# Optimization experiments

Hardware: AMD Instinct MI355X
Metric: run time of the kernel (lower is better)

Reference implementation:

```python
import jax, jax.numpy as jnp
import numpy as np

MARGIN = 1.0  # init kwarg margin=1; hard_mining=False path


def setup_inputs() -> dict:
    key = jax.random.key(0)
    k1, k2 = jax.random.split(key)
    inputs = jax.random.normal(k1, (4096, 128), dtype=jnp.float32)
    targets = jax.random.randint(k2, (4096,), 0, 64, dtype=jnp.int64)
    return {"inputs": inputs, "targets": targets}


def reference(inputs, targets):
    n = inputs.shape[0]
    # squared pairwise distances: ||xi||^2 + ||xj||^2 - 2 xi.xj, relu'd then sqrt
    sq = jnp.sum(inputs * inputs, axis=1)                      # [n]
    d2 = jnp.maximum(sq[:, None] + sq[None, :] - 2.0 * (inputs @ inputs.T), 0.0)
    nz = d2 > 0
    dist = jnp.where(nz, jnp.sqrt(jnp.where(nz, d2, 1.0)), 0.0)  # safe sqrt, [n,n]

    eye = jnp.eye(n, dtype=bool)
    same = targets[:, None] == targets[None, :]
    pos_mask = same & ~eye            # positive pairs, diag removed
    neg_mask = ~same                  # negative pairs

    # torch code gathers neg_dist[i].nonzero(): negatives with nonzero distance
    neg_valid = neg_mask & (dist != 0.0)
    row_neg = jnp.sum(jnp.where(neg_valid, jnp.exp(MARGIN - dist), 0.0), axis=1)  # [n]

    # loop runs over upper-triangular positive pairs (diag already excluded)
    idx = jnp.arange(n)
    triu_pos = pos_mask & (idx[:, None] < idx[None, :])
    J = jnp.log(row_neg[:, None] + row_neg[None, :]) + dist    # Jij_heat
    contrib = jnp.where(triu_pos, jax.nn.relu(J) ** 2, 0.0)

    len_p = jnp.sum(pos_mask).astype(inputs.dtype)             # count over FULL pos_mask
    return jnp.sum(contrib) / len_p
```

## Files before the change

### kernel.cpp

```cpp
#include <hip/hip_runtime.h>
#include <hip/hip_bf16.h>
#include <math.h>

typedef short short8 __attribute__((ext_vector_type(8)));
typedef float f32x4 __attribute__((ext_vector_type(4)));

#define NROW 4096
#define DIM  128
#define NCLS 64
#define CCAP 512
#define MAXM 128

typedef __attribute__((address_space(3))) unsigned lds_u32;
typedef const __attribute__((address_space(1))) unsigned glb_u32;

__device__ __forceinline__ void gload16(const void* g, void* lds) {
    __builtin_amdgcn_global_load_lds((glb_u32*)g, (lds_u32*)lds, 16, 0, 0);
}

__device__ __forceinline__ unsigned short f2bf(float f) {
    unsigned u = __builtin_bit_cast(unsigned, f);
    unsigned r = (u + 0x7fffu + ((u >> 16) & 1u)) >> 16;
    return (unsigned short)r;
}

__global__ __launch_bounds__(256) void prep_kernel(const float* __restrict__ X,
        unsigned short* __restrict__ Xb, float* __restrict__ sq,
        float* __restrict__ rn, float* __restrict__ acc,
        unsigned* __restrict__ tick, int* __restrict__ ccnt)
{
    int t = threadIdx.x;
    int row = blockIdx.x * 8 + (t >> 5);
    int c = t & 31;
    float4 v = *reinterpret_cast<const float4*>(X + (size_t)row * DIM + c * 4);
    float p = v.x * v.x + v.y * v.y + v.z * v.z + v.w * v.w;
    p += __shfl_xor(p, 16, 32);
    p += __shfl_xor(p, 8, 32);
    p += __shfl_xor(p, 4, 32);
    p += __shfl_xor(p, 2, 32);
    p += __shfl_xor(p, 1, 32);
    ushort4 h;
    h.x = f2bf(v.x); h.y = f2bf(v.y); h.z = f2bf(v.z); h.w = f2bf(v.w);
    *reinterpret_cast<ushort4*>(Xb + (size_t)row * DIM + c * 4) = h;
    if (c == 0) { sq[row] = p; rn[row] = 0.0f; }
    if (blockIdx.x == 0) {
        if (t < NCLS) ccnt[t] = 0;
        if (t == 64) { acc[0] = 0.0f; acc[1] = 0.0f; }
        if (t == 65) tick[0] = 0u;
    }
}

__global__ __launch_bounds__(256) void rowneg_kernel(
        const unsigned short* __restrict__ Xb, const float* __restrict__ sq,
        const int* __restrict__ tgt, float* __restrict__ rn,
        int* __restrict__ ccnt, int* __restrict__ list)
{
    const int bi = blockIdx.y, bj = blockIdx.x;
    if (bj < bi) return;
    const int gib = bi * 64, gjb = bj * 64;

    __shared__ __align__(16) unsigned short tA[64 * 128];
    __shared__ __align__(16) unsigned short tB[64 * 128];
    __shared__ float s_sqi[64], s_sqj[64];
    __shared__ float s_cacc[4][64];
    __shared__ int   s_ti[64], s_tj[64];

    const int t = threadIdx.x;
    const int w = t >> 6, l = t & 63, lr = l & 15, lg = l >> 4;

    #pragma unroll
    for (int k = 0; k < 4; ++k) {
        int q = w * 4 + k;
        int row = q * 4 + (l >> 4);
        int c16 = l & 15;
        int sc = c16 ^ (row & 7);
        gload16(Xb + (size_t)(gib + row) * DIM + sc * 8, &tA[q * 512]);
        gload16(Xb + (size_t)(gjb + row) * DIM + sc * 8, &tB[q * 512]);
    }
    if (t < 64)       { s_sqi[t] = sq[gib + t]; s_ti[t] = tgt[gib + t]; }
    else if (t < 128) { int u = t - 64; s_sqj[u] = sq[gjb + u]; s_tj[u] = tgt[gjb + u]; }
    if (bi == bj && t >= 128 && t < 192) {
        int row = gib + (t - 128);
        int cls = tgt[row];
        int p = atomicAdd(&ccnt[cls], 1);
        if (p < CCAP) list[cls * CCAP + p] = row;
    }
    __syncthreads();

    const int arow = w * 16 + lr;
    f32x4 C[4] = {};
    #pragma unroll
    for (int ks = 0; ks < 4; ++ks) {
        int c = ks * 4 + lg;
        short8 a = *reinterpret_cast<const short8*>(&tA[arow * 128 + ((c ^ (arow & 7)) * 8)]);
        #pragma unroll
        for (int fj = 0; fj < 4; ++fj) {
            int brow = fj * 16 + lr;
            short8 b = *reinterpret_cast<const short8*>(&tB[brow * 128 + ((c ^ (brow & 7)) * 8)]);
            C[fj] = __builtin_amdgcn_mfma_f32_16x16x32_bf16(a, b, C[fj], 0, 0, 0);
        }
    }

    const int ibase = w * 16 + lg * 4;
    float sqi[4]; int ti[4];
    #pragma unroll
    for (int r = 0; r < 4; ++r) { sqi[r] = s_sqi[ibase + r]; ti[r] = s_ti[ibase + r]; }

    float racc[4] = {0.f, 0.f, 0.f, 0.f};
    float cacc[4] = {0.f, 0.f, 0.f, 0.f};
    #pragma unroll
    for (int fj = 0; fj < 4; ++fj) {
        int jl = fj * 16 + lr;
        float sqj = s_sqj[jl];
        int   tj  = s_tj[jl];
        int   gj  = gjb + jl;
        #pragma unroll
        for (int r = 0; r < 4; ++r) {
            int gi = gib + ibase + r;
            float d2 = fmaxf(sqi[r] + sqj - 2.0f * C[fj][r], 0.0f);
            float dist = __builtin_amdgcn_sqrtf(d2);
            float e = __expf(1.0f - dist);
            bool valid = (gi < gj) && (ti[r] != tj) && (d2 > 0.0f);
            e = valid ? e : 0.0f;
            racc[r] += e;
            cacc[fj] += e;
        }
    }

    #pragma unroll
    for (int r = 0; r < 4; ++r) {
        racc[r] += __shfl_xor(racc[r], 1);
        racc[r] += __shfl_xor(racc[r], 2);
        racc[r] += __shfl_xor(racc[r], 4);
        racc[r] += __shfl_xor(racc[r], 8);
    }
    if (lr == 0) {
        #pragma unroll
        for (int r = 0; r < 4; ++r) atomicAdd(&rn[gib + ibase + r], racc[r]);
    }
    #pragma unroll
    for (int fj = 0; fj < 4; ++fj) {
        cacc[fj] += __shfl_xor(cacc[fj], 16);
        cacc[fj] += __shfl_xor(cacc[fj], 32);
    }
    if (lg == 0) {
        #pragma unroll
        for (int fj = 0; fj < 4; ++fj) s_cacc[w][fj * 16 + lr] = cacc[fj];
    }
    __syncthreads();
    if (t < 64) {
        float cs = s_cacc[0][t] + s_cacc[1][t] + s_cacc[2][t] + s_cacc[3][t];
        if (cs != 0.0f) atomicAdd(&rn[gjb + t], cs);
    }
}

__global__ __launch_bounds__(256) void loss_kernel(
        const unsigned short* __restrict__ Xb, const float* __restrict__ X,
        const float* __restrict__ sq, const float* __restrict__ rn,
        const int* __restrict__ ccnt, const int* __restrict__ list,
        float* __restrict__ acc, unsigned* __restrict__ tick, float* __restrict__ out)
{
    const int c = blockIdx.x;
    int m = ccnt[c]; if (m > CCAP) m = CCAP;
    const int mm = m < MAXM ? m : MAXM;
    const int nfj = (mm + 15) >> 4;

    __shared__ __align__(16) unsigned short tX[MAXM * DIM];
    __shared__ float sqg[MAXM], rng[MAXM];
    __shared__ int   s_idx[MAXM];
    __shared__ float s_red[16];

    const int t = threadIdx.x;
    const int w = t >> 6, l = t & 63, lr = l & 15, lg = l >> 4;

    if (t < MAXM) s_idx[t] = (t < mm) ? list[c * CCAP + t] : 0;
    __syncthreads();

    if (t < MAXM) {
        int ri = s_idx[t];
        sqg[t] = (t < mm) ? sq[ri] : 0.0f;
        rng[t] = (t < mm) ? rn[ri] : 0.0f;
    }
    #pragma unroll
    for (int k = 0; k < 8; ++k) {
        int q = w * 8 + k;
        int row = q * 4 + (l >> 4);
        if (row < ((mm + 3) & ~3)) {
            int c16 = l & 15;
            int sc = c16 ^ (row & 7);
            gload16(Xb + (size_t)s_idx[row] * DIM + sc * 8, &tX[q * 512]);
        }
    }
    __syncthreads();

    f32x4 C[2][8] = {};
    #pragma unroll
    for (int ks = 0; ks < 4; ++ks) {
        int cb = ks * 4 + lg;
        short8 a[2], b[8];
        #pragma unroll
        for (int fi = 0; fi < 2; ++fi) {
            int row = w * 32 + fi * 16 + lr;
            a[fi] = *reinterpret_cast<const short8*>(&tX[row * DIM + ((cb ^ (row & 7)) * 8)]);
        }
        #pragma unroll
        for (int fj = 0; fj < 8; ++fj) {
            int row = fj * 16 + lr;
            b[fj] = *reinterpret_cast<const short8*>(&tX[row * DIM + ((cb ^ (row & 7)) * 8)]);
        }
        #pragma unroll
        for (int fi = 0; fi < 2; ++fi) {
            if (w * 32 + fi * 16 < mm) {
                #pragma unroll
                for (int fj = 0; fj < 8; ++fj)
                    if (fj < nfj)
                        C[fi][fj] = __builtin_amdgcn_mfma_f32_16x16x32_bf16(a[fi], b[fj], C[fi][fj], 0, 0, 0);
            }
        }
    }

    float csum = 0.0f, cpairs = 0.0f;
    #pragma unroll
    for (int fi = 0; fi < 2; ++fi) {
        if (w * 32 + fi * 16 < mm) {
            #pragma unroll
            for (int fj = 0; fj < 8; ++fj) {
                if (fj < nfj) {
                    int q = fj * 16 + lr;
                    #pragma unroll
                    for (int r = 0; r < 4; ++r) {
                        int p = w * 32 + fi * 16 + lg * 4 + r;
                        if (q < mm && p < q) {
                            float d2 = fmaxf(sqg[p] + sqg[q] - 2.0f * C[fi][fj][r], 0.0f);
                            float dist = __builtin_amdgcn_sqrtf(d2);
                            float J = __logf(rng[p] + rng[q]) + dist;
                            if (J > 0.0f) csum += J * J;
                            cpairs += 1.0f;
                        }
                    }
                }
            }
        }
    }

    if (m > MAXM) {
        for (int q = MAXM; q < m; ++q) {
            int rq = list[c * CCAP + q];
            float sqq = sq[rq], rnq = rn[rq];
            for (int p = t; p < q; p += 256) {
                int rp = list[c * CCAP + p];
                const float4* xa = reinterpret_cast<const float4*>(X + (size_t)rp * DIM);
                const float4* xb = reinterpret_cast<const float4*>(X + (size_t)rq * DIM);
                float d = 0.0f;
                for (int k = 0; k < 32; ++k) {
                    float4 av = xa[k], bv = xb[k];
                    d += av.x * bv.x + av.y * bv.y + av.z * bv.z + av.w * bv.w;
                }
                float d2 = fmaxf(sq[rp] + sqq - 2.0f * d, 0.0f);
                float dist = __builtin_amdgcn_sqrtf(d2);
                float J = __logf(rn[rp] + rnq) + dist;
                if (J > 0.0f) csum += J * J;
                cpairs += 1.0f;
            }
        }
    }

    #pragma unroll
    for (int mr = 1; mr < 64; mr <<= 1) {
        csum   += __shfl_xor(csum, mr);
        cpairs += __shfl_xor(cpairs, mr);
    }
    if (l == 0) { s_red[w] = csum; s_red[8 + w] = cpairs; }
    __syncthreads();
    if (t == 0) {
        float bs = s_red[0] + s_red[1] + s_red[2] + s_red[3];
        float bc = s_red[8] + s_red[9] + s_red[10] + s_red[11];
        atomicAdd(&acc[0], bs);
        atomicAdd(&acc[1], bc);
        __threadfence();
        unsigned old = atomicAdd(tick, 1u);
        if (old == NCLS - 1) {
            float s  = atomicAdd(&acc[0], 0.0f);
            float n2 = atomicAdd(&acc[1], 0.0f);
            out[0] = s / (2.0f * n2);
        }
    }
}

extern "C" void kernel_launch(void* const* d_in, const int* in_sizes, int n_in,
                              void* d_out, int out_size, void* d_ws, size_t ws_size,
                              hipStream_t stream)
{
    const float* X  = (const float*)d_in[0];
    const int* tgt  = (const int*)d_in[1];
    float* out      = (float*)d_out;

    char* ws = (char*)d_ws;
    unsigned short* Xb = (unsigned short*)ws;
    float* sq   = (float*)(ws + (size_t)NROW * DIM * 2);
    float* rn   = sq + NROW;
    float* acc  = rn + NROW;
    unsigned* tick = (unsigned*)(acc + 4);
    int* ccnt   = (int*)(tick + 4);
    int* list   = ccnt + NCLS;

    prep_kernel<<<NROW / 8, 256, 0, stream>>>(X, Xb, sq, rn, acc, tick, ccnt);
    rowneg_kernel<<<dim3(64, 64), 256, 0, stream>>>(Xb, sq, tgt, rn, ccnt, list);
    loss_kernel<<<NCLS, 256, 0, stream>>>(Xb, X, sq, rn, ccnt, list, acc, tick, out);
}
```

Before: 40.37 us.

## Use 128x128 triangular tiles for rowneg and restructure loss MFMA loop

The row-negative kernel now uses 128x128 tiles with 512 threads. It launches a compact 1D grid of upper-triangular tile pairs, decoded from the block index, instead of a 64x64 grid where half the blocks exit early. Diagonal tiles reuse the A tile rather than loading B, and each block issues fewer atomic row and column accumulations. The loss kernel computes one 16-row fragment group at a time to lower accumulator register pressure. In exchange each block needs more LDS (about 64KB) and there are fewer blocks to spread across the GPU.

```diff
diff --git a/kernel.cpp b/kernel.cpp
--- a/kernel.cpp
+++ b/kernel.cpp
@@ -10,6 +10,8 @@
 #define NCLS 64
 #define CCAP 512
 #define MAXM 128
+#define NBT  32
+#define NTILE 528
 
 typedef __attribute__((address_space(3))) unsigned lds_u32;
 typedef const __attribute__((address_space(1))) unsigned glb_u32;
@@ -50,54 +52,61 @@
     }
 }
 
-__global__ __launch_bounds__(256) void rowneg_kernel(
+__global__ __launch_bounds__(512, 4) void rowneg_kernel(
         const unsigned short* __restrict__ Xb, const float* __restrict__ sq,
         const int* __restrict__ tgt, float* __restrict__ rn,
         int* __restrict__ ccnt, int* __restrict__ list)
 {
-    const int bi = blockIdx.y, bj = blockIdx.x;
-    if (bj < bi) return;
-    const int gib = bi * 64, gjb = bj * 64;
-
-    __shared__ __align__(16) unsigned short tA[64 * 128];
-    __shared__ __align__(16) unsigned short tB[64 * 128];
-    __shared__ float s_sqi[64], s_sqj[64];
-    __shared__ float s_cacc[4][64];
-    __shared__ int   s_ti[64], s_tj[64];
-
     const int t = threadIdx.x;
     const int w = t >> 6, l = t & 63, lr = l & 15, lg = l >> 4;
 
-    #pragma unroll
-    for (int k = 0; k < 4; ++k) {
-        int q = w * 4 + k;
+    const int k = blockIdx.x;
+    int bi = (int)(32.5f - sqrtf(32.5f * 32.5f - 2.0f * (float)k));
+    if (bi < 0) bi = 0; if (bi > NBT - 1) bi = NBT - 1;
+    while (bi < NBT - 1 && ((bi + 1) * NBT - (((bi + 1) * bi) >> 1)) <= k) ++bi;
+    while (bi > 0 && (bi * NBT - ((bi * (bi - 1)) >> 1)) > k) --bi;
+    const int bj = bi + (k - (bi * NBT - ((bi * (bi - 1)) >> 1)));
+    const int gib = bi * 128, gjb = bj * 128;
+    const bool diag = (bi == bj);
+
+    __shared__ __align__(16) unsigned short tA[128 * 128];
+    __shared__ __align__(16) unsigned short tB[128 * 128];
+    __shared__ float s_sqi[128], s_sqj[128];
+    __shared__ float s_cacc[8][128];
+    __shared__ int   s_ti[128], s_tj[128];
+
+    #pragma unroll
+    for (int kk = 0; kk < 4; ++kk) {
+        int q = w * 4 + kk;
         int row = q * 4 + (l >> 4);
-        int c16 = l & 15;
-        int sc = c16 ^ (row & 7);
+        int sc = (l & 15) ^ (row & 7);
         gload16(Xb + (size_t)(gib + row) * DIM + sc * 8, &tA[q * 512]);
-        gload16(Xb + (size_t)(gjb + row) * DIM + sc * 8, &tB[q * 512]);
-    }
-    if (t < 64)       { s_sqi[t] = sq[gib + t]; s_ti[t] = tgt[gib + t]; }
-    else if (t < 128) { int u = t - 64; s_sqj[u] = sq[gjb + u]; s_tj[u] = tgt[gjb + u]; }
-    if (bi == bj && t >= 128 && t < 192) {
-        int row = gib + (t - 128);
+        if (!diag)
+            gload16(Xb + (size_t)(gjb + row) * DIM + sc * 8, &tB[q * 512]);
+    }
+    if (t < 128)      { s_sqi[t] = sq[gib + t]; s_ti[t] = tgt[gib + t]; }
+    else if (t < 256) { int u = t - 128; s_sqj[u] = sq[gjb + u]; s_tj[u] = tgt[gjb + u]; }
+    else if (diag && t < 384) {
+        int row = gib + (t - 256);
         int cls = tgt[row];
         int p = atomicAdd(&ccnt[cls], 1);
         if (p < CCAP) list[cls * CCAP + p] = row;
     }
     __syncthreads();
 
+    const unsigned short* tBp = diag ? tA : tB;
     const int arow = w * 16 + lr;
-    f32x4 C[4] = {};
+
+    f32x4 C[8] = {};
     #pragma unroll
     for (int ks = 0; ks < 4; ++ks) {
         int c = ks * 4 + lg;
         short8 a = *reinterpret_cast<const short8*>(&tA[arow * 128 + ((c ^ (arow & 7)) * 8)]);
         #pragma unroll
-        for (int fj = 0; fj < 4; ++fj) {
+        for (int fj = 0; fj < 8; ++fj) {
             int brow = fj * 16 + lr;
-            short8 b = *reinterpret_cast<const short8*>(&tB[brow * 128 + ((c ^ (brow & 7)) * 8)]);
-            C[fj] = __builtin_amdgcn_mfma_f32_16x16x32_bf16(a, b, C[fj], 0, 0, 0);
+            short8 bb = *reinterpret_cast<const short8*>(&tBp[brow * 128 + ((c ^ (brow & 7)) * 8)]);
+            C[fj] = __builtin_amdgcn_mfma_f32_16x16x32_bf16(a, bb, C[fj], 0, 0, 0);
         }
     }
 
@@ -107,9 +116,9 @@
     for (int r = 0; r < 4; ++r) { sqi[r] = s_sqi[ibase + r]; ti[r] = s_ti[ibase + r]; }
 
     float racc[4] = {0.f, 0.f, 0.f, 0.f};
-    float cacc[4] = {0.f, 0.f, 0.f, 0.f};
-    #pragma unroll
-    for (int fj = 0; fj < 4; ++fj) {
+    float cacc[8] = {0.f, 0.f, 0.f, 0.f, 0.f, 0.f, 0.f, 0.f};
+    #pragma unroll
+    for (int fj = 0; fj < 8; ++fj) {
         int jl = fj * 16 + lr;
         float sqj = s_sqj[jl];
         int   tj  = s_tj[jl];
@@ -139,17 +148,19 @@
         for (int r = 0; r < 4; ++r) atomicAdd(&rn[gib + ibase + r], racc[r]);
     }
     #pragma unroll
-    for (int fj = 0; fj < 4; ++fj) {
+    for (int fj = 0; fj < 8; ++fj) {
         cacc[fj] += __shfl_xor(cacc[fj], 16);
         cacc[fj] += __shfl_xor(cacc[fj], 32);
     }
     if (lg == 0) {
         #pragma unroll
-        for (int fj = 0; fj < 4; ++fj) s_cacc[w][fj * 16 + lr] = cacc[fj];
-    }
-    __syncthreads();
-    if (t < 64) {
-        float cs = s_cacc[0][t] + s_cacc[1][t] + s_cacc[2][t] + s_cacc[3][t];
+        for (int fj = 0; fj < 8; ++fj) s_cacc[w][fj * 16 + lr] = cacc[fj];
+    }
+    __syncthreads();
+    if (t < 128) {
+        float cs = 0.0f;
+        #pragma unroll
+        for (int ww = 0; ww < 8; ++ww) cs += s_cacc[ww][t];
         if (cs != 0.0f) atomicAdd(&rn[gjb + t], cs);
     }
 }
@@ -175,63 +186,51 @@
 
     if (t < MAXM) s_idx[t] = (t < mm) ? list[c * CCAP + t] : 0;
     __syncthreads();
-
     if (t < MAXM) {
         int ri = s_idx[t];
         sqg[t] = (t < mm) ? sq[ri] : 0.0f;
         rng[t] = (t < mm) ? rn[ri] : 0.0f;
     }
     #pragma unroll
-    for (int k = 0; k < 8; ++k) {
-        int q = w * 8 + k;
+    for (int kk = 0; kk < 8; ++kk) {
+        int q = w * 8 + kk;
         int row = q * 4 + (l >> 4);
         if (row < ((mm + 3) & ~3)) {
-            int c16 = l & 15;
-            int sc = c16 ^ (row & 7);
+            int sc = (l & 15) ^ (row & 7);
             gload16(Xb + (size_t)s_idx[row] * DIM + sc * 8, &tX[q * 512]);
         }
     }
     __syncthreads();
 
-    f32x4 C[2][8] = {};
-    #pragma unroll
-    for (int ks = 0; ks < 4; ++ks) {
-        int cb = ks * 4 + lg;
-        short8 a[2], b[8];
-        #pragma unroll
-        for (int fi = 0; fi < 2; ++fi) {
-            int row = w * 32 + fi * 16 + lr;
-            a[fi] = *reinterpret_cast<const short8*>(&tX[row * DIM + ((cb ^ (row & 7)) * 8)]);
-        }
-        #pragma unroll
-        for (int fj = 0; fj < 8; ++fj) {
-            int row = fj * 16 + lr;
-            b[fj] = *reinterpret_cast<const short8*>(&tX[row * DIM + ((cb ^ (row & 7)) * 8)]);
-        }
-        #pragma unroll
-        for (int fi = 0; fi < 2; ++fi) {
-            if (w * 32 + fi * 16 < mm) {
+    float csum = 0.0f, cpairs = 0.0f;
+    #pragma unroll
+    for (int fi = 0; fi < 2; ++fi) {
+        const int rowbase = fi * 64 + w * 16;
+        if (rowbase < mm) {
+            f32x4 C[8] = {};
+            const int arow = rowbase + lr;
+            #pragma unroll
+            for (int ks = 0; ks < 4; ++ks) {
+                int cb = ks * 4 + lg;
+                short8 a = *reinterpret_cast<const short8*>(&tX[arow * DIM + ((cb ^ (arow & 7)) * 8)]);
                 #pragma unroll
-                for (int fj = 0; fj < 8; ++fj)
-                    if (fj < nfj)
-                        C[fi][fj] = __builtin_amdgcn_mfma_f32_16x16x32_bf16(a[fi], b[fj], C[fi][fj], 0, 0, 0);
+                for (int fj = 0; fj < 8; ++fj) {
+                    if (fj < nfj) {
+                        int brow = fj * 16 + lr;
+                        short8 bb = *reinterpret_cast<const short8*>(&tX[brow * DIM + ((cb ^ (brow & 7)) * 8)]);
+                        C[fj] = __builtin_amdgcn_mfma_f32_16x16x32_bf16(a, bb, C[fj], 0, 0, 0);
+                    }
+                }
             }
-        }
-    }
-
-    float csum = 0.0f, cpairs = 0.0f;
-    #pragma unroll
-    for (int fi = 0; fi < 2; ++fi) {
-        if (w * 32 + fi * 16 < mm) {
             #pragma unroll
             for (int fj = 0; fj < 8; ++fj) {
                 if (fj < nfj) {
                     int q = fj * 16 + lr;
                     #pragma unroll
                     for (int r = 0; r < 4; ++r) {
-                        int p = w * 32 + fi * 16 + lg * 4 + r;
+                        int p = rowbase + lg * 4 + r;
                         if (q < mm && p < q) {
-                            float d2 = fmaxf(sqg[p] + sqg[q] - 2.0f * C[fi][fj][r], 0.0f);
+                            float d2 = fmaxf(sqg[p] + sqg[q] - 2.0f * C[fj][r], 0.0f);
                             float dist = __builtin_amdgcn_sqrtf(d2);
                             float J = __logf(rng[p] + rng[q]) + dist;
                             if (J > 0.0f) csum += J * J;
@@ -252,8 +251,8 @@
                 const float4* xa = reinterpret_cast<const float4*>(X + (size_t)rp * DIM);
                 const float4* xb = reinterpret_cast<const float4*>(X + (size_t)rq * DIM);
                 float d = 0.0f;
-                for (int k = 0; k < 32; ++k) {
-                    float4 av = xa[k], bv = xb[k];
+                for (int kq = 0; kq < 32; ++kq) {
+                    float4 av = xa[kq], bv = xb[kq];
                     d += av.x * bv.x + av.y * bv.y + av.z * bv.z + av.w * bv.w;
                 }
                 float d2 = fmaxf(sq[rp] + sqq - 2.0f * d, 0.0f);
@@ -305,6 +304,6 @@
     int* list   = ccnt + NCLS;
 
     prep_kernel<<<NROW / 8, 256, 0, stream>>>(X, Xb, sq, rn, acc, tick, ccnt);
-    rowneg_kernel<<<dim3(64, 64), 256, 0, stream>>>(Xb, sq, tgt, rn, ccnt, list);
+    rowneg_kernel<<<NTILE, 512, 0, stream>>>(Xb, sq, tgt, rn, ccnt, list);
     loss_kernel<<<NCLS, 256, 0, stream>>>(Xb, X, sq, rn, ccnt, list, acc, tick, out);
 }
```

Result: slower. 42.84 us (+6.1%).

## Fuse bf16 prep into tile kernels, launch only upper-triangle tiles, split loss blocks

Applied to the files above, without the earlier changes.

Drops the separate prep kernel. The row-negative and loss kernels now read fp32 inputs directly, compute squared norms, and pack to bf16 into swizzled LDS, while a memset zeroes the workspace. The row-negative grid is reduced to the 2080 upper-triangular tiles, indexed by a triangular-number inversion, so half the blocks no longer exit early. Each class in the loss kernel is split across two blocks to add parallelism. In exchange, every tile reloads and converts fp32 rows, which doubles global read bytes per tile and drops the async global-to-LDS load path.

```diff
diff --git a/kernel.cpp b/kernel.cpp
--- a/kernel.cpp
+++ b/kernel.cpp
@@ -10,13 +10,8 @@
 #define NCLS 64
 #define CCAP 512
 #define MAXM 128
-
-typedef __attribute__((address_space(3))) unsigned lds_u32;
-typedef const __attribute__((address_space(1))) unsigned glb_u32;
-
-__device__ __forceinline__ void gload16(const void* g, void* lds) {
-    __builtin_amdgcn_global_load_lds((glb_u32*)g, (lds_u32*)lds, 16, 0, 0);
-}
+#define NBT  64
+#define NTILE 2080
 
 __device__ __forceinline__ unsigned short f2bf(float f) {
     unsigned u = __builtin_bit_cast(unsigned, f);
@@ -24,39 +19,28 @@
     return (unsigned short)r;
 }
 
-__global__ __launch_bounds__(256) void prep_kernel(const float* __restrict__ X,
-        unsigned short* __restrict__ Xb, float* __restrict__ sq,
-        float* __restrict__ rn, float* __restrict__ acc,
-        unsigned* __restrict__ tick, int* __restrict__ ccnt)
+__device__ __forceinline__ short8 pack8(const float4& a, const float4& b) {
+    short8 h;
+    h[0] = (short)f2bf(a.x); h[1] = (short)f2bf(a.y);
+    h[2] = (short)f2bf(a.z); h[3] = (short)f2bf(a.w);
+    h[4] = (short)f2bf(b.x); h[5] = (short)f2bf(b.y);
+    h[6] = (short)f2bf(b.z); h[7] = (short)f2bf(b.w);
+    return h;
+}
+
+__global__ __launch_bounds__(256, 4) void rowneg_kernel(
+        const float* __restrict__ X, const int* __restrict__ tgt,
+        float* __restrict__ rn, int* __restrict__ ccnt, int* __restrict__ list)
 {
-    int t = threadIdx.x;
-    int row = blockIdx.x * 8 + (t >> 5);
-    int c = t & 31;
-    float4 v = *reinterpret_cast<const float4*>(X + (size_t)row * DIM + c * 4);
-    float p = v.x * v.x + v.y * v.y + v.z * v.z + v.w * v.w;
-    p += __shfl_xor(p, 16, 32);
-    p += __shfl_xor(p, 8, 32);
-    p += __shfl_xor(p, 4, 32);
-    p += __shfl_xor(p, 2, 32);
-    p += __shfl_xor(p, 1, 32);
-    ushort4 h;
-    h.x = f2bf(v.x); h.y = f2bf(v.y); h.z = f2bf(v.z); h.w = f2bf(v.w);
-    *reinterpret_cast<ushort4*>(Xb + (size_t)row * DIM + c * 4) = h;
-    if (c == 0) { sq[row] = p; rn[row] = 0.0f; }
-    if (blockIdx.x == 0) {
-        if (t < NCLS) ccnt[t] = 0;
-        if (t == 64) { acc[0] = 0.0f; acc[1] = 0.0f; }
-        if (t == 65) tick[0] = 0u;
-    }
-}
-
-__global__ __launch_bounds__(256) void rowneg_kernel(
-        const unsigned short* __restrict__ Xb, const float* __restrict__ sq,
-        const int* __restrict__ tgt, float* __restrict__ rn,
-        int* __restrict__ ccnt, int* __restrict__ list)
-{
-    const int bi = blockIdx.y, bj = blockIdx.x;
-    if (bj < bi) return;
+    const int t = threadIdx.x;
+    const int w = t >> 6, l = t & 63, lr = l & 15, lg = l >> 4;
+
+    const int k = blockIdx.x;
+    int bi = (int)(64.5f - sqrtf(64.5f * 64.5f - 2.0f * (float)k));
+    if (bi < 0) bi = 0; if (bi > NBT - 1) bi = NBT - 1;
+    while (bi < NBT - 1 && ((bi + 1) * NBT - (((bi + 1) * bi) >> 1)) <= k) ++bi;
+    while (bi > 0 && (bi * NBT - ((bi * (bi - 1)) >> 1)) > k) --bi;
+    const int bj = bi + (k - (bi * NBT - ((bi * (bi - 1)) >> 1)));
     const int gib = bi * 64, gjb = bj * 64;
 
     __shared__ __align__(16) unsigned short tA[64 * 128];
@@ -65,21 +49,34 @@
     __shared__ float s_cacc[4][64];
     __shared__ int   s_ti[64], s_tj[64];
 
-    const int t = threadIdx.x;
-    const int w = t >> 6, l = t & 63, lr = l & 15, lg = l >> 4;
-
-    #pragma unroll
-    for (int k = 0; k < 4; ++k) {
-        int q = w * 4 + k;
-        int row = q * 4 + (l >> 4);
-        int c16 = l & 15;
-        int sc = c16 ^ (row & 7);
-        gload16(Xb + (size_t)(gib + row) * DIM + sc * 8, &tA[q * 512]);
-        gload16(Xb + (size_t)(gjb + row) * DIM + sc * 8, &tB[q * 512]);
-    }
-    if (t < 64)       { s_sqi[t] = sq[gib + t]; s_ti[t] = tgt[gib + t]; }
-    else if (t < 128) { int u = t - 64; s_sqj[u] = sq[gjb + u]; s_tj[u] = tgt[gjb + u]; }
-    if (bi == bj && t >= 128 && t < 192) {
+    {
+        const int row  = t >> 1;
+        const int half = t & 1;
+        const int grow = (row < 64) ? (gib + row) : (gjb + row - 64);
+        const float4* src = reinterpret_cast<const float4*>(X + (size_t)grow * DIM + half * 64);
+        float4 buf[16];
+        #pragma unroll
+        for (int q = 0; q < 16; ++q) buf[q] = src[q];
+        float p = 0.0f;
+        #pragma unroll
+        for (int q = 0; q < 16; ++q)
+            p += buf[q].x * buf[q].x + buf[q].y * buf[q].y + buf[q].z * buf[q].z + buf[q].w * buf[q].w;
+        p += __shfl_xor(p, 1);
+        unsigned short* dst = (row < 64) ? tA : tB;
+        const int lrow = row & 63;
+        #pragma unroll
+        for (int q = 0; q < 8; ++q) {
+            int c16 = half * 8 + q;
+            *reinterpret_cast<short8*>(&dst[lrow * 128 + ((c16 ^ (lrow & 7)) * 8)]) =
+                pack8(buf[2 * q], buf[2 * q + 1]);
+        }
+        if (half == 0) {
+            if (row < 64) s_sqi[row] = p; else s_sqj[row - 64] = p;
+        }
+    }
+    if (t < 64)       s_ti[t] = tgt[gib + t];
+    else if (t < 128) s_tj[t - 64] = tgt[gjb + t - 64];
+    else if (bi == bj && t < 192) {
         int row = gib + (t - 128);
         int cls = tgt[row];
         int p = atomicAdd(&ccnt[cls], 1);
@@ -96,8 +93,8 @@
         #pragma unroll
         for (int fj = 0; fj < 4; ++fj) {
             int brow = fj * 16 + lr;
-            short8 b = *reinterpret_cast<const short8*>(&tB[brow * 128 + ((c ^ (brow & 7)) * 8)]);
-            C[fj] = __builtin_amdgcn_mfma_f32_16x16x32_bf16(a, b, C[fj], 0, 0, 0);
+            short8 bb = *reinterpret_cast<const short8*>(&tB[brow * 128 + ((c ^ (brow & 7)) * 8)]);
+            C[fj] = __builtin_amdgcn_mfma_f32_16x16x32_bf16(a, bb, C[fj], 0, 0, 0);
         }
     }
 
@@ -155,12 +152,12 @@
 }
 
 __global__ __launch_bounds__(256) void loss_kernel(
-        const unsigned short* __restrict__ Xb, const float* __restrict__ X,
-        const float* __restrict__ sq, const float* __restrict__ rn,
+        const float* __restrict__ X, const float* __restrict__ rn,
         const int* __restrict__ ccnt, const int* __restrict__ list,
         float* __restrict__ acc, unsigned* __restrict__ tick, float* __restrict__ out)
 {
-    const int c = blockIdx.x;
+    const int c = blockIdx.x >> 1;
+    const int h = blockIdx.x & 1;
     int m = ccnt[c]; if (m > CCAP) m = CCAP;
     const int mm = m < MAXM ? m : MAXM;
     const int nfj = (mm + 15) >> 4;
@@ -173,65 +170,67 @@
     const int t = threadIdx.x;
     const int w = t >> 6, l = t & 63, lr = l & 15, lg = l >> 4;
 
+    float csum = 0.0f, cpairs = 0.0f;
+
+    if (h == 1 && mm <= 64) goto tickout;
+
     if (t < MAXM) s_idx[t] = (t < mm) ? list[c * CCAP + t] : 0;
     __syncthreads();
 
-    if (t < MAXM) {
-        int ri = s_idx[t];
-        sqg[t] = (t < mm) ? sq[ri] : 0.0f;
-        rng[t] = (t < mm) ? rn[ri] : 0.0f;
-    }
-    #pragma unroll
-    for (int k = 0; k < 8; ++k) {
-        int q = w * 8 + k;
-        int row = q * 4 + (l >> 4);
-        if (row < ((mm + 3) & ~3)) {
-            int c16 = l & 15;
-            int sc = c16 ^ (row & 7);
-            gload16(Xb + (size_t)s_idx[row] * DIM + sc * 8, &tX[q * 512]);
+    {
+        const int row  = t >> 1;
+        const int half = t & 1;
+        if (row < mm) {
+            const int ri = s_idx[row];
+            const float4* src = reinterpret_cast<const float4*>(X + (size_t)ri * DIM + half * 64);
+            float4 buf[16];
+            #pragma unroll
+            for (int q = 0; q < 16; ++q) buf[q] = src[q];
+            float p = 0.0f;
+            #pragma unroll
+            for (int q = 0; q < 16; ++q)
+                p += buf[q].x * buf[q].x + buf[q].y * buf[q].y + buf[q].z * buf[q].z + buf[q].w * buf[q].w;
+            p += __shfl_xor(p, 1);
+            #pragma unroll
+            for (int q = 0; q < 8; ++q) {
+                int c16 = half * 8 + q;
+                *reinterpret_cast<short8*>(&tX[row * 128 + ((c16 ^ (row & 7)) * 8)]) =
+                    pack8(buf[2 * q], buf[2 * q + 1]);
+            }
+            if (half == 0) { sqg[row] = p; rng[row] = rn[ri]; }
+        } else if (half == 0 && row < MAXM) {
+            sqg[row] = 0.0f; rng[row] = 0.0f;
         }
     }
     __syncthreads();
 
-    f32x4 C[2][8] = {};
-    #pragma unroll
-    for (int ks = 0; ks < 4; ++ks) {
-        int cb = ks * 4 + lg;
-        short8 a[2], b[8];
-        #pragma unroll
-        for (int fi = 0; fi < 2; ++fi) {
-            int row = w * 32 + fi * 16 + lr;
-            a[fi] = *reinterpret_cast<const short8*>(&tX[row * DIM + ((cb ^ (row & 7)) * 8)]);
-        }
-        #pragma unroll
-        for (int fj = 0; fj < 8; ++fj) {
-            int row = fj * 16 + lr;
-            b[fj] = *reinterpret_cast<const short8*>(&tX[row * DIM + ((cb ^ (row & 7)) * 8)]);
-        }
-        #pragma unroll
-        for (int fi = 0; fi < 2; ++fi) {
-            if (w * 32 + fi * 16 < mm) {
+    {
+        const int rowbase = h * 64 + w * 16;
+        if (rowbase < mm) {
+            f32x4 C[8] = {};
+            const int arow = rowbase + lr;
+            #pragma unroll
+            for (int ks = 0; ks < 4; ++ks) {
+                int cb = ks * 4 + lg;
+                short8 a = *reinterpret_cast<const short8*>(&tX[arow * DIM + ((cb ^ (arow & 7)) * 8)]);
                 #pragma unroll
-                for (int fj = 0; fj < 8; ++fj)
-                    if (fj < nfj)
-                        C[fi][fj] = __builtin_amdgcn_mfma_f32_16x16x32_bf16(a[fi], b[fj], C[fi][fj], 0, 0, 0);
+                for (int fj = 0; fj < 8; ++fj) {
+                    if (fj < nfj) {
+                        int brow = fj * 16 + lr;
+                        short8 bb = *reinterpret_cast<const short8*>(&tX[brow * DIM + ((cb ^ (brow & 7)) * 8)]);
+                        C[fj] = __builtin_amdgcn_mfma_f32_16x16x32_bf16(a, bb, C[fj], 0, 0, 0);
+                    }
+                }
             }
-        }
-    }
-
-    float csum = 0.0f, cpairs = 0.0f;
-    #pragma unroll
-    for (int fi = 0; fi < 2; ++fi) {
-        if (w * 32 + fi * 16 < mm) {
             #pragma unroll
             for (int fj = 0; fj < 8; ++fj) {
                 if (fj < nfj) {
                     int q = fj * 16 + lr;
                     #pragma unroll
                     for (int r = 0; r < 4; ++r) {
-                        int p = w * 32 + fi * 16 + lg * 4 + r;
+                        int p = rowbase + lg * 4 + r;
                         if (q < mm && p < q) {
-                            float d2 = fmaxf(sqg[p] + sqg[q] - 2.0f * C[fi][fj][r], 0.0f);
+                            float d2 = fmaxf(sqg[p] + sqg[q] - 2.0f * C[fj][r], 0.0f);
                             float dist = __builtin_amdgcn_sqrtf(d2);
                             float J = __logf(rng[p] + rng[q]) + dist;
                             if (J > 0.0f) csum += J * J;
@@ -241,45 +240,54 @@
                 }
             }
         }
-    }
-
-    if (m > MAXM) {
-        for (int q = MAXM; q < m; ++q) {
-            int rq = list[c * CCAP + q];
-            float sqq = sq[rq], rnq = rn[rq];
-            for (int p = t; p < q; p += 256) {
-                int rp = list[c * CCAP + p];
-                const float4* xa = reinterpret_cast<const float4*>(X + (size_t)rp * DIM);
+
+        if (h == 0 && m > MAXM) {
+            for (int q = MAXM; q < m; ++q) {
+                int rq = list[c * CCAP + q];
                 const float4* xb = reinterpret_cast<const float4*>(X + (size_t)rq * DIM);
-                float d = 0.0f;
-                for (int k = 0; k < 32; ++k) {
-                    float4 av = xa[k], bv = xb[k];
-                    d += av.x * bv.x + av.y * bv.y + av.z * bv.z + av.w * bv.w;
+                float sqq = 0.0f;
+                for (int kq = 0; kq < 32; ++kq) {
+                    float4 bv = xb[kq];
+                    sqq += bv.x * bv.x + bv.y * bv.y + bv.z * bv.z + bv.w * bv.w;
                 }
-                float d2 = fmaxf(sq[rp] + sqq - 2.0f * d, 0.0f);
-                float dist = __builtin_amdgcn_sqrtf(d2);
-                float J = __logf(rn[rp] + rnq) + dist;
-                if (J > 0.0f) csum += J * J;
-                cpairs += 1.0f;
+                float rnq = rn[rq];
+                for (int p = t; p < q; p += 256) {
+                    int rp = list[c * CCAP + p];
+                    const float4* xa = reinterpret_cast<const float4*>(X + (size_t)rp * DIM);
+                    float d = 0.0f, sqp = 0.0f;
+                    for (int kq = 0; kq < 32; ++kq) {
+                        float4 av = xa[kq], bv = xb[kq];
+                        d += av.x * bv.x + av.y * bv.y + av.z * bv.z + av.w * bv.w;
+                        sqp += av.x * av.x + av.y * av.y + av.z * av.z + av.w * av.w;
+                    }
+                    float d2 = fmaxf(sqp + sqq - 2.0f * d, 0.0f);
+                    float dist = __builtin_amdgcn_sqrtf(d2);
+                    float J = __logf(rn[rp] + rnq) + dist;
+                    if (J > 0.0f) csum += J * J;
+                    cpairs += 1.0f;
+                }
             }
         }
-    }
-
-    #pragma unroll
-    for (int mr = 1; mr < 64; mr <<= 1) {
-        csum   += __shfl_xor(csum, mr);
-        cpairs += __shfl_xor(cpairs, mr);
-    }
-    if (l == 0) { s_red[w] = csum; s_red[8 + w] = cpairs; }
-    __syncthreads();
+
+        #pragma unroll
+        for (int mr = 1; mr < 64; mr <<= 1) {
+            csum   += __shfl_xor(csum, mr);
+            cpairs += __shfl_xor(cpairs, mr);
+        }
+        if (l == 0) { s_red[w] = csum; s_red[8 + w] = cpairs; }
+        __syncthreads();
+        if (t == 0 && (s_red[0] + s_red[1] + s_red[2] + s_red[3] != 0.0f ||
+                       s_red[8] + s_red[9] + s_red[10] + s_red[11] != 0.0f)) {
+            atomicAdd(&acc[0], s_red[0] + s_red[1] + s_red[2] + s_red[3]);
+            atomicAdd(&acc[1], s_red[8] + s_red[9] + s_red[10] + s_red[11]);
+        }
+    }
+
+tickout:
+    __threadfence();
     if (t == 0) {
-        float bs = s_red[0] + s_red[1] + s_red[2] + s_red[3];
-        float bc = s_red[8] + s_red[9] + s_red[10] + s_red[11];
-        atomicAdd(&acc[0], bs);
-        atomicAdd(&acc[1], bc);
-        __threadfence();
         unsigned old = atomicAdd(tick, 1u);
-        if (old == NCLS - 1) {
+        if (old == 2 * NCLS - 1) {
             float s  = atomicAdd(&acc[0], 0.0f);
             float n2 = atomicAdd(&acc[1], 0.0f);
             out[0] = s / (2.0f * n2);
@@ -296,15 +304,13 @@
     float* out      = (float*)d_out;
 
     char* ws = (char*)d_ws;
-    unsigned short* Xb = (unsigned short*)ws;
-    float* sq   = (float*)(ws + (size_t)NROW * DIM * 2);
-    float* rn   = sq + NROW;
-    float* acc  = rn + NROW;
-    unsigned* tick = (unsigned*)(acc + 4);
-    int* ccnt   = (int*)(tick + 4);
-    int* list   = ccnt + NCLS;
-
-    prep_kernel<<<NROW / 8, 256, 0, stream>>>(X, Xb, sq, rn, acc, tick, ccnt);
-    rowneg_kernel<<<dim3(64, 64), 256, 0, stream>>>(Xb, sq, tgt, rn, ccnt, list);
-    loss_kernel<<<NCLS, 256, 0, stream>>>(Xb, X, sq, rn, ccnt, list, acc, tick, out);
-}
+    float*    rn   = (float*)ws;
+    float*    acc  = rn + NROW;
+    unsigned* tick = (unsigned*)(acc + 2);
+    int*      ccnt = (int*)(tick + 2);
+    int*      list = ccnt + NCLS;
+
+    hipMemsetAsync(ws, 0, (size_t)((char*)list - ws), stream);
+    rowneg_kernel<<<NTILE, 256, 0, stream>>>(X, tgt, rn, ccnt, list);
+    loss_kernel<<<2 * NCLS, 256, 0, stream>>>(X, rn, ccnt, list, acc, tick, out);
+}
```

Result: slower. 54.69 us (+35.5%).
